# Kernel tuning notes

Measured on AMD Instinct MI355X. Metric: run time of the kernel, lower is better.

## Reference

```python
import jax, jax.numpy as jnp
import numpy as np

FIELD_NUM = 40
EMBED_DIM = 64
BATCH = 2048

# pair indices matching itertools.combinations(range(F), 2) order
_I, _J = np.triu_indices(FIELD_NUM, k=1)
PAIR_I = jnp.asarray(_I)
PAIR_J = jnp.asarray(_J)


def setup_inputs() -> dict:
    key = jax.random.key(0)
    k1, k2 = jax.random.split(key)
    inputs = jax.random.normal(k1, (BATCH, FIELD_NUM, EMBED_DIM), dtype=jnp.float32)
    # glorot_normal for square [D, D] weight: std = sqrt(2 / (D + D)) = sqrt(1/D)
    w = jax.random.normal(k2, (EMBED_DIM, EMBED_DIM), dtype=jnp.float32) * (1.0 / EMBED_DIM) ** 0.5
    return {"inputs": inputs, "w": w}


def reference(inputs, w):
    # inputs: [B, F, D], w: [D, D]
    # bilinear_type='all': p_{ij} = (v_i @ W) * v_j for all i<j, concat on feature axis
    xw = jnp.einsum("bfd,de->bfe", inputs, w)          # [B, F, D] (one GEMM, shared W)
    p = xw[:, PAIR_I, :] * inputs[:, PAIR_J, :]          # [B, P, D], P = F*(F-1)/2
    B = inputs.shape[0]
    return p.reshape(B, -1)                               # [B, P*D] == tf.concat(p, axis=1)
```

## Files before the change

### kernel.cpp

```cpp
#include <hip/hip_runtime.h>

#define FNUM 40
#define DIM  64
#define NPAIR 780
#define BLOCK 256
#define IN4   (FNUM * DIM / 4)
#define OUT4  (NPAIR * DIM / 4)

typedef float f32x4 __attribute__((ext_vector_type(4)));

__global__ __launch_bounds__(BLOCK)
void bilinear_fused(const float* __restrict__ in,
                    const float* __restrict__ w,
                    float* __restrict__ out)
{
    __shared__ float sIn[FNUM * DIM];
    __shared__ float sXW[FNUM * DIM];
    __shared__ unsigned char sPi[NPAIR];
    __shared__ unsigned char sPj[NPAIR];

    const int tid  = threadIdx.x;
    const int b    = blockIdx.x;
    const int lane = tid & 63;
    const int wv   = tid >> 6;

    const f32x4* in4 = (const f32x4*)in + (size_t)b * IN4;
    f32x4* sIn4 = (f32x4*)sIn;
    for (int k = tid; k < IN4; k += BLOCK) sIn4[k] = in4[k];

    if (tid < FNUM) {
        int i = tid;
        int off = i * (2 * FNUM - 1 - i) / 2;
        for (int j = i + 1; j < FNUM; ++j) {
            sPi[off] = (unsigned char)i;
            sPj[off] = (unsigned char)j;
            ++off;
        }
    }

    float wcol[DIM];
    #pragma unroll
    for (int d = 0; d < DIM; ++d) wcol[d] = w[d * DIM + lane];

    __syncthreads();

    for (int r = 0; r < 10; ++r) {
        int f = wv * 10 + r;
        float rin = sIn[f * DIM + lane];
        float acc = 0.f;
        #pragma unroll
        for (int d = 0; d < DIM; ++d) {
            float bv = __uint_as_float(
                __builtin_amdgcn_readlane(__float_as_uint(rin), d));
            acc = fmaf(bv, wcol[d], acc);
        }
        sXW[f * DIM + lane] = acc;
    }

    __syncthreads();

    const f32x4* sXW4 = (const f32x4*)sXW;
    f32x4* out4 = (f32x4*)out + (size_t)b * OUT4;
    for (int idx = tid; idx < OUT4; idx += BLOCK) {
        int p = idx >> 4;
        int q = idx & 15;
        int i = sPi[p];
        int j = sPj[p];
        f32x4 a = sXW4[i * 16 + q];
        f32x4 v = sIn4[j * 16 + q];
        f32x4 o = a * v;
        __builtin_nontemporal_store(o, &out4[idx]);
    }
}

extern "C" void kernel_launch(void* const* d_in, const int* in_sizes, int n_in,
                              void* d_out, int out_size, void* d_ws, size_t ws_size,
                              hipStream_t stream)
{
    const float* in = (const float*)d_in[0];
    const float* w  = (const float*)d_in[1];
    float* out = (float*)d_out;

    bilinear_fused<<<2048, BLOCK, 0, stream>>>(in, w, out);
}
```

Before: 420.4 us.

## Drop input staging in LDS, register-block GEMM, compute pair indices incrementally

The input is no longer staged in shared memory. Each wave computes 10 rows of xW by reading the input rows and W directly from global memory, keeping 10 accumulators instead of a 64-entry W column in registers. The output loop drops the pair lookup tables and advances the (i,j) pair indices incrementally, reading v_j from global memory, which should hit in cache. Lower register and LDS use, together with the launch-bounds hint of 8, aims for higher occupancy. The cost is repeated global/L1 reads in place of LDS reads.

New measurement: 452.9 us. 1.08x slower.

```diff
diff --git a/kernel.cpp b/kernel.cpp
--- a/kernel.cpp
+++ b/kernel.cpp
@@ -9,68 +9,72 @@
 
 typedef float f32x4 __attribute__((ext_vector_type(4)));
 
-__global__ __launch_bounds__(BLOCK)
+__global__ __launch_bounds__(BLOCK, 8)
 void bilinear_fused(const float* __restrict__ in,
                     const float* __restrict__ w,
                     float* __restrict__ out)
 {
-    __shared__ float sIn[FNUM * DIM];
     __shared__ float sXW[FNUM * DIM];
-    __shared__ unsigned char sPi[NPAIR];
-    __shared__ unsigned char sPj[NPAIR];
 
     const int tid  = threadIdx.x;
     const int b    = blockIdx.x;
     const int lane = tid & 63;
-    const int wv   = tid >> 6;
+    const int wv   = __builtin_amdgcn_readfirstlane(tid >> 6);
 
-    const f32x4* in4 = (const f32x4*)in + (size_t)b * IN4;
-    f32x4* sIn4 = (f32x4*)sIn;
-    for (int k = tid; k < IN4; k += BLOCK) sIn4[k] = in4[k];
+    {
+        const float* __restrict__ inw = in + (size_t)b * (FNUM * DIM) + (size_t)(wv * 10) * DIM;
+        float acc[10];
+        #pragma unroll
+        for (int r = 0; r < 10; ++r) acc[r] = 0.f;
 
-    if (tid < FNUM) {
-        int i = tid;
-        int off = i * (2 * FNUM - 1 - i) / 2;
-        for (int j = i + 1; j < FNUM; ++j) {
-            sPi[off] = (unsigned char)i;
-            sPj[off] = (unsigned char)j;
-            ++off;
+        #pragma unroll 4
+        for (int d = 0; d < DIM; ++d) {
+            float wd = w[d * DIM + lane];
+            #pragma unroll
+            for (int r = 0; r < 10; ++r)
+                acc[r] = fmaf(inw[r * DIM + d], wd, acc[r]);
         }
-    }
-
-    float wcol[DIM];
-    #pragma unroll
-    for (int d = 0; d < DIM; ++d) wcol[d] = w[d * DIM + lane];
-
-    __syncthreads();
-
-    for (int r = 0; r < 10; ++r) {
-        int f = wv * 10 + r;
-        float rin = sIn[f * DIM + lane];
-        float acc = 0.f;
         #pragma unroll
-        for (int d = 0; d < DIM; ++d) {
-            float bv = __uint_as_float(
-                __builtin_amdgcn_readlane(__float_as_uint(rin), d));
-            acc = fmaf(bv, wcol[d], acc);
-        }
-        sXW[f * DIM + lane] = acc;
+        for (int r = 0; r < 10; ++r)
+            sXW[(wv * 10 + r) * DIM + lane] = acc[r];
     }
 
     __syncthreads();
 
-    const f32x4* sXW4 = (const f32x4*)sXW;
-    f32x4* out4 = (f32x4*)out + (size_t)b * OUT4;
-    for (int idx = tid; idx < OUT4; idx += BLOCK) {
-        int p = idx >> 4;
-        int q = idx & 15;
-        int i = sPi[p];
-        int j = sPj[p];
+    const f32x4* __restrict__ sXW4 = (const f32x4*)sXW;
+    const f32x4* __restrict__ in4  = (const f32x4*)in  + (size_t)b * IN4;
+    f32x4*       __restrict__ out4 = (f32x4*)out + (size_t)b * OUT4;
+
+    const int q = tid & 15;
+    int i = 0;
+    int j = 1 + (tid >> 4);
+
+    #define ADV()                                          \
+        do {                                               \
+            j += 16;                                       \
+            while (j >= FNUM && i < FNUM) {                \
+                j = (j - FNUM) + (i + 2);                  \
+                ++i;                                       \
+            }                                              \
+        } while (0)
+
+    #pragma unroll 4
+    for (int k = 0; k < 48; ++k) {
+        int idx = tid + k * BLOCK;
         f32x4 a = sXW4[i * 16 + q];
-        f32x4 v = sIn4[j * 16 + q];
-        f32x4 o = a * v;
-        __builtin_nontemporal_store(o, &out4[idx]);
+        f32x4 v = in4[j * 16 + q];
+        __builtin_nontemporal_store(a * v, &out4[idx]);
+        ADV();
     }
+    {
+        int idx = tid + 48 * BLOCK;
+        if (idx < OUT4) {
+            f32x4 a = sXW4[i * 16 + q];
+            f32x4 v = in4[j * 16 + q];
+            __builtin_nontemporal_store(a * v, &out4[idx]);
+        }
+    }
+    #undef ADV
 }
 
 extern "C" void kernel_launch(void* const* d_in, const int* in_sizes, int n_in,
```
